# Optimization experiments

Measured on AMD Instinct MI355X. Metric: run time of the kernel, lower is better.

Reference implementation:

```python
import jax, jax.numpy as jnp
import numpy as np

B, T, E = 8, 2048, 512  # batch, seq_len, dim (single head, head_dim == dim)
EPS = 1e-3


def setup_inputs() -> dict:
    key = jax.random.key(0)
    ks = jax.random.split(key, 6)
    s = E ** -0.5  # scale proj weights like nn.Linear init so exp(k) stays finite
    return {
        "x": jax.random.normal(ks[0], (B, E, T), jnp.float32),
        "toep_weight": jax.random.normal(ks[1], (1, T), jnp.float32),
        "q_w": jax.random.normal(ks[2], (E, E), jnp.float32) * s,
        "q_b": jnp.zeros((E,), jnp.float32),
        "k_w": jax.random.normal(ks[3], (E, E), jnp.float32) * s,
        "k_b": jnp.zeros((E,), jnp.float32),
        "v_w": jax.random.normal(ks[4], (E, E), jnp.float32) * s,
        "v_b": jnp.zeros((E,), jnp.float32),
        "o_w": jax.random.normal(ks[5], (E, E), jnp.float32) * s,
        "o_b": jnp.zeros((E,), jnp.float32),
    }


def reference(x, toep_weight, q_w, q_b, k_w, k_b, v_w, v_b, o_w, o_b):
    # x: (B, E, T) -> (B, T, E)
    xt = jnp.transpose(x, (0, 2, 1))
    q = xt @ q_w.T + q_b
    k = xt @ k_w.T + k_b
    v = xt @ v_w.T + v_b
    # feature maps: softmax(q) * d^-1/2 , exp(k); v scaled by per-position Toeplitz weight
    q = jax.nn.softmax(q, axis=-1) * (E ** -0.5)
    k = jnp.exp(k)
    v = v * toep_weight[0][:, None]  # (T,1) broadcast over (B,T,E)
    # causal linear attention: running outer-product state S (B,E,E) and key-sum z (B,E)
    qs = jnp.transpose(q, (1, 0, 2))  # (T, B, E)
    kk = jnp.transpose(k, (1, 0, 2))
    vv = jnp.transpose(v, (1, 0, 2))

    def step(carry, inp):
        S, z = carry
        qt, kt, vt = inp  # each (B, E)
        S = S + kt[:, :, None] * vt[:, None, :]  # cumulative k v^T
        z = z + kt                                # cumulative key sum
        d = jnp.maximum(jnp.sum(z * qt, axis=-1), EPS)  # clamp then reciprocal
        out = jnp.einsum('bd,bde->be', qt, S) / d[:, None]
        return (S, z), out

    S0 = jnp.zeros((B, E, E), q.dtype)
    z0 = jnp.zeros((B, E), q.dtype)
    _, outs = jax.lax.scan(step, (S0, z0), (qs, kk, vv))  # outs: (T, B, E)
    attn = jnp.transpose(outs, (1, 0, 2))  # (B, T, E)
    return attn @ o_w.T + o_b
```

## Files before the change

### kernel.cpp

```cpp
#include <hip/hip_runtime.h>
#include <hip/hip_bf16.h>
#include <math.h>
#include <stdint.h>

#define B_ 8
#define T_ 2048
#define E_ 512
#define CCH 256
#define NC_ 8
#define EPS_ 1e-3f
#define QSCALE 0.044194173824159216f

typedef __attribute__((ext_vector_type(8))) short short8;
typedef __attribute__((ext_vector_type(4))) float f32x4;
typedef __hip_bfloat16 bf16_t;

__device__ __forceinline__ short f2bs(float x) {
    bf16_t h = __float2bfloat16(x);
    return __builtin_bit_cast(short, h);
}

__device__ __forceinline__ void async16(const void* g, void* l) {
    __builtin_amdgcn_global_load_lds(
        (const __attribute__((address_space(1))) unsigned int*)(unsigned long long)(uintptr_t)g,
        (__attribute__((address_space(3))) unsigned int*)(unsigned int)(uintptr_t)l,
        16, 0, 0);
}

__device__ __forceinline__ void gemm128(const short* __restrict__ Ag, int lda,
                                        const short* __restrict__ Bg, int ldb, int K,
                                        short* Al, short* Bl, f32x4 acc[4][4],
                                        int wm, int wn, int wq, int lane) {
    int m16 = lane & 15, quad = lane >> 4;
    int r16 = lane & 15, c4 = (lane >> 4) * 8;
    for (int k0 = 0; k0 < K; k0 += 32) {
        __syncthreads();
        #pragma unroll
        for (int w = 0; w < 2; ++w) {
            int win = wq + w * 4;
            int R = win * 16;
            async16(Ag + (size_t)(R + r16) * lda + k0 + c4, Al + win * 512);
            async16(Bg + (size_t)(R + r16) * ldb + k0 + c4, Bl + win * 512);
        }
        __syncthreads();
        short8 a[4], b[4];
        #pragma unroll
        for (int i = 0; i < 4; ++i)
            a[i] = *(const short8*)(Al + (wm + i * 16) * 32 + quad * 128 + m16 * 8);
        #pragma unroll
        for (int i = 0; i < 4; ++i)
            b[i] = *(const short8*)(Bl + (wn + i * 16) * 32 + quad * 128 + m16 * 8);
        #pragma unroll
        for (int i = 0; i < 4; ++i)
            #pragma unroll
            for (int j = 0; j < 4; ++j)
                acc[i][j] = __builtin_amdgcn_mfma_f32_16x16x32_bf16(a[i], b[j], acc[i][j], 0, 0, 0);
    }
}

#define GEMM_PROLOG \
    int tid = threadIdx.x, lane = tid & 63, wq = tid >> 6; \
    int wm = (wq & 1) * 64, wn = (wq >> 1) * 64; \
    int m16 = lane & 15, quad = lane >> 4; \
    (void)tid; \
    f32x4 acc[4][4]; \
    { f32x4 zz = {0.f, 0.f, 0.f, 0.f}; \
      for (int i = 0; i < 4; ++i) for (int j = 0; j < 4; ++j) acc[i][j] = zz; }

__global__ void prep_kernel(const float* __restrict__ qw, const float* __restrict__ kw,
                            const float* __restrict__ vw, const float* __restrict__ ow,
                            short* __restrict__ wbf,
                            const float* __restrict__ x, short* __restrict__ xbf) {
    int bid = blockIdx.x;
    int tid = threadIdx.x;
    if (bid < 512) {
        size_t idx8 = ((size_t)bid * 256 + tid) * 8;
        int sel = (int)(idx8 >> 18);
        size_t off = idx8 & ((1u << 18) - 1);
        const float* src = sel == 0 ? qw : sel == 1 ? kw : sel == 2 ? vw : ow;
        const float4* sp = (const float4*)(src + off);
        float4 a = sp[0], b = sp[1];
        short8 g;
        g[0] = f2bs(a.x); g[1] = f2bs(a.y); g[2] = f2bs(a.z); g[3] = f2bs(a.w);
        g[4] = f2bs(b.x); g[5] = f2bs(b.y); g[6] = f2bs(b.z); g[7] = f2bs(b.w);
        *(short8*)(wbf + idx8) = g;
        return;
    }
    bid -= 512;
    __shared__ __align__(16) float S[64][68];
    int t0 = (bid & 31) * 64, e0 = ((bid >> 5) & 7) * 64, b = bid >> 8;
    const float* src = x + ((size_t)b * E_ + e0) * T_ + t0;
    short* dst = xbf + ((size_t)b * T_ + t0) * E_ + e0;
    #pragma unroll
    for (int p = 0; p < 2; ++p) {
        int el = p * 32 + (tid >> 3), tc = (tid & 7) * 8;
        const float4* sp = (const float4*)(src + (size_t)el * T_ + tc);
        *(float4*)&S[el][tc] = sp[0];
        *(float4*)&S[el][tc + 4] = sp[1];
    }
    __syncthreads();
    #pragma unroll
    for (int p = 0; p < 2; ++p) {
        int tl = p * 32 + (tid >> 3), ec = (tid & 7) * 8;
        short8 g;
        #pragma unroll
        for (int j = 0; j < 8; ++j) g[j] = f2bs(S[ec + j][tl]);
        *(short8*)(dst + (size_t)tl * E_ + ec) = g;
    }
}

__global__ void transpose_bf_kernel(const short* __restrict__ k, const short* __restrict__ v,
                                    short* __restrict__ kT, short* __restrict__ vT) {
    __shared__ __align__(16) short S[64][72];
    int tid = threadIdx.x;
    int t0 = blockIdx.x * 64, e0 = blockIdx.y * 64;
    int b = blockIdx.z >> 1, which = blockIdx.z & 1;
    const short* src = (which ? v : k) + ((size_t)b * T_ + t0) * E_ + e0;
    short* dst = (which ? vT : kT) + ((size_t)b * E_ + e0) * T_ + t0;
    #pragma unroll
    for (int p = 0; p < 2; ++p) {
        int tl = p * 32 + (tid >> 3), ec = (tid & 7) * 8;
        *(short8*)&S[tl][ec] = *(const short8*)(src + (size_t)tl * E_ + ec);
    }
    __syncthreads();
    #pragma unroll
    for (int p = 0; p < 2; ++p) {
        int er = p * 32 + (tid >> 3), tc = (tid & 7) * 8;
        short8 g;
        #pragma unroll
        for (int j = 0; j < 8; ++j) g[j] = S[tc + j][er];
        *(short8*)(dst + (size_t)er * T_ + tc) = g;
    }
}

__global__ __launch_bounds__(256) void proj_qkv_kernel(
    const short* __restrict__ xbf, const short* __restrict__ wbf,
    const float* __restrict__ qb, const float* __restrict__ kb, const float* __restrict__ vb,
    const float* __restrict__ toep,
    bf16_t* __restrict__ qraw, bf16_t* __restrict__ kout, bf16_t* __restrict__ vout) {
    __shared__ __align__(16) short Al[128 * 32], Bl[128 * 32];
    GEMM_PROLOG
    int t0 = blockIdx.x * 128, i0 = blockIdx.y * 128;
    int b = blockIdx.z / 3, sel = blockIdx.z % 3;
    const short* Ag = xbf + ((size_t)b * T_ + t0) * E_;
    const short* Bg = wbf + (size_t)sel * E_ * E_ + (size_t)i0 * E_;
    gemm128(Ag, E_, Bg, E_, E_, Al, Bl, acc, wm, wn, wq, lane);
    const float* bias = (sel == 0) ? qb : (sel == 1) ? kb : vb;
    #pragma unroll
    for (int mt = 0; mt < 4; ++mt)
        #pragma unroll
        for (int r = 0; r < 4; ++r) {
            int t = t0 + wm + mt * 16 + quad * 4 + r;
            size_t rowoff = ((size_t)b * T_ + t) * E_;
            float tw = toep[t];
            #pragma unroll
            for (int nt = 0; nt < 4; ++nt) {
                int col = i0 + wn + nt * 16 + m16;
                float vv = acc[mt][nt][r] + bias[col];
                if (sel == 0) qraw[rowoff + col] = __float2bfloat16(vv);
                else if (sel == 1) kout[rowoff + col] = __float2bfloat16(expf(vv));
                else vout[rowoff + col] = __float2bfloat16(vv * tw);
            }
        }
}

__global__ void softmax_ksum_kernel(const bf16_t* __restrict__ qraw, bf16_t* __restrict__ qbf,
                                    const bf16_t* __restrict__ k, float* __restrict__ ks) {
    int bid = blockIdx.x, tid = threadIdx.x;
    if (bid >= B_ * T_) {
        int r = bid - B_ * T_;
        int bc = r >> 1, b = bc >> 3, c = bc & 7;
        int e = (r & 1) * 256 + tid;
        const bf16_t* kp = k + ((size_t)b * T_ + (size_t)c * CCH) * E_ + e;
        float s = 0.f;
        for (int t = 0; t < CCH; ++t) s += __bfloat162float(kp[(size_t)t * E_]);
        ks[(size_t)bc * E_ + e] = s;
        return;
    }
    __shared__ float red[256];
    const bf16_t* p = qraw + (size_t)bid * E_;
    float v0 = __bfloat162float(p[tid]), v1 = __bfloat162float(p[tid + 256]);
    red[tid] = fmaxf(v0, v1);
    __syncthreads();
    for (int s = 128; s > 0; s >>= 1) { if (tid < s) red[tid] = fmaxf(red[tid], red[tid + s]); __syncthreads(); }
    float m = red[0];
    __syncthreads();
    float e0 = expf(v0 - m), e1 = expf(v1 - m);
    red[tid] = e0 + e1;
    __syncthreads();
    for (int s = 128; s > 0; s >>= 1) { if (tid < s) red[tid] += red[tid + s]; __syncthreads(); }
    float inv = QSCALE / red[0];
    qbf[(size_t)bid * E_ + tid] = __float2bfloat16(e0 * inv);
    qbf[(size_t)bid * E_ + tid + 256] = __float2bfloat16(e1 * inv);
}

__global__ __launch_bounds__(256) void kvp_kernel(
    const short* __restrict__ vT, const short* __restrict__ kT, bf16_t* __restrict__ KV,
    const short* __restrict__ qbf, const short* __restrict__ kbf, bf16_t* __restrict__ P) {
    __shared__ __align__(16) short Al[128 * 32], Bl[128 * 32];
    int bid = blockIdx.x;
    if (bid < 1024) {
        GEMM_PROLOG
        int ev0 = (bid & 3) * 128, ek0 = ((bid >> 2) & 3) * 128;
        int bc = bid >> 4, b = bc >> 3, c = bc & 7;
        const short* Ag = vT + ((size_t)b * E_ + ev0) * T_ + c * CCH;
        const short* Bg = kT + ((size_t)b * E_ + ek0) * T_ + c * CCH;
        gemm128(Ag, T_, Bg, T_, CCH, Al, Bl, acc, wm, wn, wq, lane);
        #pragma unroll
        for (int mt = 0; mt < 4; ++mt)
            #pragma unroll
            for (int r = 0; r < 4; ++r) {
                int ev = ev0 + wm + mt * 16 + quad * 4 + r;
                #pragma unroll
                for (int nt = 0; nt < 4; ++nt) {
                    int ek = ek0 + wn + nt * 16 + m16;
                    KV[((size_t)bc * E_ + ev) * E_ + ek] = __float2bfloat16(acc[mt][nt][r]);
                }
            }
        return;
    }
    bid -= 1024;
    int tj0 = (bid & 1) * 128, ti0 = ((bid >> 1) & 1) * 128;
    int bc = bid >> 2, b = bc >> 3, c = bc & 7;
    short* Pp = (short*)P + (size_t)bc * CCH * CCH;
    if (tj0 > ti0) {
        short8 z8 = {0, 0, 0, 0, 0, 0, 0, 0};
        for (int i = threadIdx.x; i < 128 * 128 / 8; i += 256) {
            int row = i >> 4, colc = (i * 8) & 127;
            *(short8*)(Pp + (size_t)(ti0 + row) * CCH + tj0 + colc) = z8;
        }
        return;
    }
    GEMM_PROLOG
    const short* Ag = qbf + ((size_t)b * T_ + c * CCH + ti0) * E_;
    const short* Bg = kbf + ((size_t)b * T_ + c * CCH + tj0) * E_;
    gemm128(Ag, E_, Bg, E_, E_, Al, Bl, acc, wm, wn, wq, lane);
    #pragma unroll
    for (int mt = 0; mt < 4; ++mt)
        #pragma unroll
        for (int r = 0; r < 4; ++r) {
            int row = ti0 + wm + mt * 16 + quad * 4 + r;
            #pragma unroll
            for (int nt = 0; nt < 4; ++nt) {
                int col = tj0 + wn + nt * 16 + m16;
                float vv = (col <= row) ? acc[mt][nt][r] : 0.f;
                ((bf16_t*)Pp)[(size_t)row * CCH + col] = __float2bfloat16(vv);
            }
        }
}

__global__ void scan2_kernel(bf16_t* __restrict__ KV, float* __restrict__ ks) {
    size_t bid = blockIdx.x;
    if (bid < 8192) {
        size_t gid = bid * 256 + threadIdx.x;
        size_t b = gid >> 18, idx = gid & ((1u << 18) - 1);
        bf16_t* p = KV + b * ((size_t)NC_ * E_ * E_) + idx;
        float run = 0.f;
        for (int c = 0; c < NC_; ++c) {
            float t = __bfloat162float(*p);
            *p = __float2bfloat16(run);
            run += t;
            p += (size_t)E_ * E_;
        }
        return;
    }
    int gid = (int)(bid - 8192) * 256 + threadIdx.x;
    int b = gid >> 9, idx = gid & (E_ - 1);
    float run = 0.f;
    float* p = ks + (size_t)b * NC_ * E_ + idx;
    for (int c = 0; c < NC_; ++c) { float t = *p; *p = run; run += t; p += E_; }
}

__global__ void denom_kernel(const bf16_t* __restrict__ qbf, const float* __restrict__ z,
                             const bf16_t* __restrict__ P, float* __restrict__ invd) {
    __shared__ float red[256];
    int row = blockIdx.x, tid = threadIdx.x;
    int b = row >> 11, t = row & (T_ - 1);
    int c = t >> 8, tl = t & 255;
    const bf16_t* qr = qbf + (size_t)row * E_;
    const float* zr = z + ((size_t)(b * NC_ + c)) * E_;
    const bf16_t* Pr = P + (((size_t)(b * NC_ + c)) * CCH + tl) * CCH;
    float s = __bfloat162float(qr[tid]) * zr[tid]
            + __bfloat162float(qr[tid + 256]) * zr[tid + 256]
            + __bfloat162float(Pr[tid]);
    red[tid] = s;
    __syncthreads();
    for (int st = 128; st > 0; st >>= 1) { if (tid < st) red[tid] += red[tid + st]; __syncthreads(); }
    if (tid == 0) invd[row] = 1.f / fmaxf(red[0], EPS_);
}

__global__ __launch_bounds__(256) void attnout_kernel(
    const short* __restrict__ qbf, const short* __restrict__ KV,
    const short* __restrict__ P, const short* __restrict__ vT,
    const float* __restrict__ invd, bf16_t* __restrict__ attn) {
    __shared__ __align__(16) short Al[128 * 32], Bl[128 * 32];
    GEMM_PROLOG
    int t0 = blockIdx.x * 128, i0 = blockIdx.y * 128, b = blockIdx.z;
    int c = t0 >> 8, tl0 = t0 & 255, bc = b * NC_ + c;
    gemm128(qbf + ((size_t)b * T_ + t0) * E_, E_,
            KV + ((size_t)bc * E_ + i0) * E_, E_, E_, Al, Bl, acc, wm, wn, wq, lane);
    gemm128(P + ((size_t)bc * CCH + tl0) * CCH, CCH,
            vT + ((size_t)b * E_ + i0) * T_ + c * CCH, T_, CCH, Al, Bl, acc, wm, wn, wq, lane);
    #pragma unroll
    for (int mt = 0; mt < 4; ++mt)
        #pragma unroll
        for (int r = 0; r < 4; ++r) {
            int t = t0 + wm + mt * 16 + quad * 4 + r;
            float sc = invd[(size_t)b * T_ + t];
            #pragma unroll
            for (int nt = 0; nt < 4; ++nt) {
                int col = i0 + wn + nt * 16 + m16;
                attn[((size_t)b * T_ + t) * E_ + col] = __float2bfloat16(acc[mt][nt][r] * sc);
            }
        }
}

__global__ __launch_bounds__(256) void outproj_kernel(
    const short* __restrict__ attn, const short* __restrict__ wbf_o,
    const float* __restrict__ ob, float* __restrict__ out) {
    __shared__ __align__(16) short Al[128 * 32], Bl[128 * 32];
    GEMM_PROLOG
    int t0 = blockIdx.x * 128, i0 = blockIdx.y * 128, b = blockIdx.z;
    gemm128(attn + ((size_t)b * T_ + t0) * E_, E_,
            wbf_o + (size_t)i0 * E_, E_, E_, Al, Bl, acc, wm, wn, wq, lane);
    #pragma unroll
    for (int mt = 0; mt < 4; ++mt)
        #pragma unroll
        for (int r = 0; r < 4; ++r) {
            int t = t0 + wm + mt * 16 + quad * 4 + r;
            #pragma unroll
            for (int nt = 0; nt < 4; ++nt) {
                int col = i0 + wn + nt * 16 + m16;
                out[((size_t)b * T_ + t) * E_ + col] = acc[mt][nt][r] + ob[col];
            }
        }
}

extern "C" void kernel_launch(void* const* d_in, const int* in_sizes, int n_in,
                              void* d_out, int out_size, void* d_ws, size_t ws_size,
                              hipStream_t stream) {
    const float* x    = (const float*)d_in[0];
    const float* toep = (const float*)d_in[1];
    const float* q_w  = (const float*)d_in[2];
    const float* q_b  = (const float*)d_in[3];
    const float* k_w  = (const float*)d_in[4];
    const float* k_b  = (const float*)d_in[5];
    const float* v_w  = (const float*)d_in[6];
    const float* v_b  = (const float*)d_in[7];
    const float* o_w  = (const float*)d_in[8];
    const float* o_b  = (const float*)d_in[9];

    const size_t NTE = (size_t)B_ * T_ * E_;
    char* base = (char*)d_ws;
    short* xbf  = (short*)base;  base += NTE * 2;
    short* wbf  = (short*)base;  base += (size_t)4 * E_ * E_ * 2;
    short* qraw = (short*)base;  base += NTE * 2;
    short* qbf  = (short*)base;  base += NTE * 2;
    short* kbf  = (short*)base;  base += NTE * 2;
    short* vbf  = (short*)base;  base += NTE * 2;
    short* kT   = (short*)base;  base += NTE * 2;
    short* vT   = (short*)base;  base += NTE * 2;
    short* KV   = (short*)base;  base += (size_t)B_ * NC_ * E_ * E_ * 2;
    short* P    = (short*)base;  base += (size_t)B_ * NC_ * CCH * CCH * 2;
    float* ksum = (float*)base;  base += (size_t)B_ * NC_ * E_ * 4;
    float* invd = (float*)base;  base += (size_t)B_ * T_ * 4;
    short* attn = xbf;
    float* out  = (float*)d_out;

    dim3 blk(256);
    prep_kernel<<<dim3(2560), blk, 0, stream>>>(q_w, k_w, v_w, o_w, wbf, x, xbf);
    proj_qkv_kernel<<<dim3(16, 4, 24), blk, 0, stream>>>(
        xbf, wbf, q_b, k_b, v_b, toep, (bf16_t*)qraw, (bf16_t*)kbf, (bf16_t*)vbf);
    softmax_ksum_kernel<<<dim3(B_ * T_ + 128), blk, 0, stream>>>(
        (const bf16_t*)qraw, (bf16_t*)qbf, (const bf16_t*)kbf, ksum);
    transpose_bf_kernel<<<dim3(32, 8, 16), blk, 0, stream>>>(kbf, vbf, kT, vT);
    kvp_kernel<<<dim3(1280), blk, 0, stream>>>(
        vT, kT, (bf16_t*)KV, qbf, kbf, (bf16_t*)P);
    scan2_kernel<<<dim3(8208), blk, 0, stream>>>((bf16_t*)KV, ksum);
    denom_kernel<<<dim3(B_ * T_), blk, 0, stream>>>(
        (const bf16_t*)qbf, ksum, (const bf16_t*)P, invd);
    attnout_kernel<<<dim3(16, 4, 8), blk, 0, stream>>>(
        qbf, KV, P, vT, invd, (bf16_t*)attn);
    outproj_kernel<<<dim3(16, 4, 8), blk, 0, stream>>>(
        attn, wbf + (size_t)3 * E_ * E_, o_b, out);
}
```

Before: 310.9 us.

## Double-buffer GEMM LDS tiles and vectorize the chunk-prefix scan

Result: no change. 308.2 us (-0.9%).

```diff
diff --git a/kernel.cpp b/kernel.cpp
--- a/kernel.cpp
+++ b/kernel.cpp
@@ -19,6 +19,10 @@
     bf16_t h = __float2bfloat16(x);
     return __builtin_bit_cast(short, h);
 }
+__device__ __forceinline__ float bs2f(short s) {
+    bf16_t h = __builtin_bit_cast(bf16_t, s);
+    return __bfloat162float(h);
+}
 
 __device__ __forceinline__ void async16(const void* g, void* l) {
     __builtin_amdgcn_global_load_lds(
@@ -29,32 +33,45 @@
 
 __device__ __forceinline__ void gemm128(const short* __restrict__ Ag, int lda,
                                         const short* __restrict__ Bg, int ldb, int K,
-                                        short* Al, short* Bl, f32x4 acc[4][4],
+                                        short* L, f32x4 acc[4][4],
                                         int wm, int wn, int wq, int lane) {
     int m16 = lane & 15, quad = lane >> 4;
-    int r16 = lane & 15, c4 = (lane >> 4) * 8;
-    for (int k0 = 0; k0 < K; k0 += 32) {
+    int r16 = lane & 15, c4 = quad * 8;
+    int nstep = K >> 5;
+    __syncthreads();
+    #pragma unroll
+    for (int w = 0; w < 2; ++w) {
+        int win = wq + w * 4;
+        async16(Ag + (size_t)(win * 16 + r16) * lda + c4, L + win * 512);
+        async16(Bg + (size_t)(win * 16 + r16) * ldb + c4, L + 4096 + win * 512);
+    }
+    for (int i = 0; i < nstep; ++i) {
+        int cur = (i & 1) << 13;
+        int nxt = 8192 - cur;
         __syncthreads();
-        #pragma unroll
-        for (int w = 0; w < 2; ++w) {
-            int win = wq + w * 4;
-            int R = win * 16;
-            async16(Ag + (size_t)(R + r16) * lda + k0 + c4, Al + win * 512);
-            async16(Bg + (size_t)(R + r16) * ldb + k0 + c4, Bl + win * 512);
-        }
-        __syncthreads();
+        if (i + 1 < nstep) {
+            int k0 = (i + 1) << 5;
+            #pragma unroll
+            for (int w = 0; w < 2; ++w) {
+                int win = wq + w * 4;
+                async16(Ag + (size_t)(win * 16 + r16) * lda + k0 + c4, L + nxt + win * 512);
+                async16(Bg + (size_t)(win * 16 + r16) * ldb + k0 + c4, L + nxt + 4096 + win * 512);
+            }
+        }
+        const short* Ac = L + cur;
+        const short* Bc = L + cur + 4096;
         short8 a[4], b[4];
         #pragma unroll
-        for (int i = 0; i < 4; ++i)
-            a[i] = *(const short8*)(Al + (wm + i * 16) * 32 + quad * 128 + m16 * 8);
-        #pragma unroll
-        for (int i = 0; i < 4; ++i)
-            b[i] = *(const short8*)(Bl + (wn + i * 16) * 32 + quad * 128 + m16 * 8);
-        #pragma unroll
-        for (int i = 0; i < 4; ++i)
+        for (int t = 0; t < 4; ++t)
+            a[t] = *(const short8*)(Ac + (wm + t * 16) * 32 + quad * 128 + m16 * 8);
+        #pragma unroll
+        for (int t = 0; t < 4; ++t)
+            b[t] = *(const short8*)(Bc + (wn + t * 16) * 32 + quad * 128 + m16 * 8);
+        #pragma unroll
+        for (int t = 0; t < 4; ++t)
             #pragma unroll
             for (int j = 0; j < 4; ++j)
-                acc[i][j] = __builtin_amdgcn_mfma_f32_16x16x32_bf16(a[i], b[j], acc[i][j], 0, 0, 0);
+                acc[t][j] = __builtin_amdgcn_mfma_f32_16x16x32_bf16(a[t], b[j], acc[t][j], 0, 0, 0);
     }
 }
 
@@ -138,13 +155,13 @@
     const float* __restrict__ qb, const float* __restrict__ kb, const float* __restrict__ vb,
     const float* __restrict__ toep,
     bf16_t* __restrict__ qraw, bf16_t* __restrict__ kout, bf16_t* __restrict__ vout) {
-    __shared__ __align__(16) short Al[128 * 32], Bl[128 * 32];
+    __shared__ __align__(16) short L[16384];
     GEMM_PROLOG
     int t0 = blockIdx.x * 128, i0 = blockIdx.y * 128;
     int b = blockIdx.z / 3, sel = blockIdx.z % 3;
     const short* Ag = xbf + ((size_t)b * T_ + t0) * E_;
     const short* Bg = wbf + (size_t)sel * E_ * E_ + (size_t)i0 * E_;
-    gemm128(Ag, E_, Bg, E_, E_, Al, Bl, acc, wm, wn, wq, lane);
+    gemm128(Ag, E_, Bg, E_, E_, L, acc, wm, wn, wq, lane);
     const float* bias = (sel == 0) ? qb : (sel == 1) ? kb : vb;
     #pragma unroll
     for (int mt = 0; mt < 4; ++mt)
@@ -197,7 +214,7 @@
 __global__ __launch_bounds__(256) void kvp_kernel(
     const short* __restrict__ vT, const short* __restrict__ kT, bf16_t* __restrict__ KV,
     const short* __restrict__ qbf, const short* __restrict__ kbf, bf16_t* __restrict__ P) {
-    __shared__ __align__(16) short Al[128 * 32], Bl[128 * 32];
+    __shared__ __align__(16) short L[16384];
     int bid = blockIdx.x;
     if (bid < 1024) {
         GEMM_PROLOG
@@ -205,7 +222,7 @@
         int bc = bid >> 4, b = bc >> 3, c = bc & 7;
         const short* Ag = vT + ((size_t)b * E_ + ev0) * T_ + c * CCH;
         const short* Bg = kT + ((size_t)b * E_ + ek0) * T_ + c * CCH;
-        gemm128(Ag, T_, Bg, T_, CCH, Al, Bl, acc, wm, wn, wq, lane);
+        gemm128(Ag, T_, Bg, T_, CCH, L, acc, wm, wn, wq, lane);
         #pragma unroll
         for (int mt = 0; mt < 4; ++mt)
             #pragma unroll
@@ -234,7 +251,7 @@
     GEMM_PROLOG
     const short* Ag = qbf + ((size_t)b * T_ + c * CCH + ti0) * E_;
     const short* Bg = kbf + ((size_t)b * T_ + c * CCH + tj0) * E_;
-    gemm128(Ag, E_, Bg, E_, E_, Al, Bl, acc, wm, wn, wq, lane);
+    gemm128(Ag, E_, Bg, E_, E_, L, acc, wm, wn, wq, lane);
     #pragma unroll
     for (int mt = 0; mt < 4; ++mt)
         #pragma unroll
@@ -249,22 +266,30 @@
         }
 }
 
-__global__ void scan2_kernel(bf16_t* __restrict__ KV, float* __restrict__ ks) {
-    size_t bid = blockIdx.x;
-    if (bid < 8192) {
-        size_t gid = bid * 256 + threadIdx.x;
-        size_t b = gid >> 18, idx = gid & ((1u << 18) - 1);
-        bf16_t* p = KV + b * ((size_t)NC_ * E_ * E_) + idx;
-        float run = 0.f;
+__global__ void scan2_kernel(short* __restrict__ KV, float* __restrict__ ks) {
+    int bid = blockIdx.x, tid = threadIdx.x;
+    if (bid < 1024) {
+        int gid = bid * 256 + tid;
+        int b = gid >> 15;
+        size_t idx = (size_t)(gid & 32767) * 8;
+        short* p = KV + (size_t)b * NC_ * E_ * E_ + idx;
+        float run[8] = {0.f, 0.f, 0.f, 0.f, 0.f, 0.f, 0.f, 0.f};
+        #pragma unroll
         for (int c = 0; c < NC_; ++c) {
-            float t = __bfloat162float(*p);
-            *p = __float2bfloat16(run);
-            run += t;
+            short8 t8 = *(short8*)p;
+            short8 o8;
+            #pragma unroll
+            for (int j = 0; j < 8; ++j) {
+                float tv = bs2f(t8[j]);
+                o8[j] = f2bs(run[j]);
+                run[j] += tv;
+            }
+            *(short8*)p = o8;
             p += (size_t)E_ * E_;
         }
         return;
     }
-    int gid = (int)(bid - 8192) * 256 + threadIdx.x;
+    int gid = (bid - 1024) * 256 + tid;
     int b = gid >> 9, idx = gid & (E_ - 1);
     float run = 0.f;
     float* p = ks + (size_t)b * NC_ * E_ + idx;
@@ -293,14 +318,14 @@
     const short* __restrict__ qbf, const short* __restrict__ KV,
     const short* __restrict__ P, const short* __restrict__ vT,
     const float* __restrict__ invd, bf16_t* __restrict__ attn) {
-    __shared__ __align__(16) short Al[128 * 32], Bl[128 * 32];
+    __shared__ __align__(16) short L[16384];
     GEMM_PROLOG
     int t0 = blockIdx.x * 128, i0 = blockIdx.y * 128, b = blockIdx.z;
     int c = t0 >> 8, tl0 = t0 & 255, bc = b * NC_ + c;
     gemm128(qbf + ((size_t)b * T_ + t0) * E_, E_,
-            KV + ((size_t)bc * E_ + i0) * E_, E_, E_, Al, Bl, acc, wm, wn, wq, lane);
+            KV + ((size_t)bc * E_ + i0) * E_, E_, E_, L, acc, wm, wn, wq, lane);
     gemm128(P + ((size_t)bc * CCH + tl0) * CCH, CCH,
-            vT + ((size_t)b * E_ + i0) * T_ + c * CCH, T_, CCH, Al, Bl, acc, wm, wn, wq, lane);
+            vT + ((size_t)b * E_ + i0) * T_ + c * CCH, T_, CCH, L, acc, wm, wn, wq, lane);
     #pragma unroll
     for (int mt = 0; mt < 4; ++mt)
         #pragma unroll
@@ -318,11 +343,11 @@
 __global__ __launch_bounds__(256) void outproj_kernel(
     const short* __restrict__ attn, const short* __restrict__ wbf_o,
     const float* __restrict__ ob, float* __restrict__ out) {
-    __shared__ __align__(16) short Al[128 * 32], Bl[128 * 32];
+    __shared__ __align__(16) short L[16384];
     GEMM_PROLOG
     int t0 = blockIdx.x * 128, i0 = blockIdx.y * 128, b = blockIdx.z;
     gemm128(attn + ((size_t)b * T_ + t0) * E_, E_,
-            wbf_o + (size_t)i0 * E_, E_, E_, Al, Bl, acc, wm, wn, wq, lane);
+            wbf_o + (size_t)i0 * E_, E_, E_, L, acc, wm, wn, wq, lane);
     #pragma unroll
     for (int mt = 0; mt < 4; ++mt)
         #pragma unroll
@@ -376,7 +401,7 @@
     transpose_bf_kernel<<<dim3(32, 8, 16), blk, 0, stream>>>(kbf, vbf, kT, vT);
     kvp_kernel<<<dim3(1280), blk, 0, stream>>>(
         vT, kT, (bf16_t*)KV, qbf, kbf, (bf16_t*)P);
-    scan2_kernel<<<dim3(8208), blk, 0, stream>>>((bf16_t*)KV, ksum);
+    scan2_kernel<<<dim3(1040), blk, 0, stream>>>(KV, ksum);
     denom_kernel<<<dim3(B_ * T_), blk, 0, stream>>>(
         (const bf16_t*)qbf, ksum, (const bf16_t*)P, invd);
     attnout_kernel<<<dim3(16, 4, 8), blk, 0, stream>>>(
```
